# Performance work log

Hardware: AMD Instinct MI355X
Metric: run time of the kernel (lower is better)

The kernel has to match this reference:

```python
import jax, jax.numpy as jnp
import numpy as np

EMBED_DIM = 128
N_CLASSES = 5
NX = 1024
NY = 1024


def setup_inputs() -> dict:
    key = jax.random.key(0)
    k1, k2 = jax.random.split(key)
    z_x = jax.random.normal(k1, (NX, EMBED_DIM), dtype=jnp.float32)
    z_y = jax.random.normal(k2, (NY, EMBED_DIM), dtype=jnp.float32)
    # Parameter init exactly as in __init__ for the L1 compare
    ex = 2 * np.sqrt(2 / np.pi) * EMBED_DIM
    var = 4 * (1 - 2 / np.pi) * EMBED_DIM
    beta_init = ex / np.sqrt(var)
    theta = jnp.ones((1, N_CLASSES - 1), dtype=jnp.float32) / np.sqrt(var)  # clamped >=0, already positive
    beta = jnp.full((N_CLASSES - 1,), beta_init, dtype=jnp.float32)
    return {"z_x": z_x, "z_y": z_y, "theta": theta, "beta": beta}


def reference(z_x, z_y, theta, beta):
    # L1 compare: s[i,j] = -sum_d |z_x[i,d] - z_y[j,d]|   -> (Nx, Ny)
    s = -jnp.sum(jnp.abs(z_x[:, None, :] - z_y[None, :, :]), axis=-1)
    # SSA: dual softmax soft alignment
    a = jax.nn.softmax(s, axis=1)  # row softmax
    b = jax.nn.softmax(s, axis=0)  # column softmax
    a = a + b - a * b
    a = a / jnp.sum(a)
    # weighted reduction -> scalar similarity
    c = jnp.sum(a * s)
    logits = c * theta + beta  # (1, n_classes-1) broadcast
    return logits.reshape(-1)
```

## Files before the change

### kernel.cpp

```cpp
#include <hip/hip_runtime.h>
#include <math.h>

#define NXC 1024
#define NYC 1024
#define DC  128
#define NCM1 4
#define NTILE 256
#define NBLKA 512

#define WS_STILE 0
#define WS_ROWP  524288
#define WS_COLP  589824
#define WS_PART  622592

typedef _Float16 half2v __attribute__((ext_vector_type(2)));
union H2U { half2v h; unsigned u; };

#if defined(__has_builtin)
#if __has_builtin(__builtin_amdgcn_fdot2)
#define HAVE_FDOT2 1
#endif
#endif

__device__ __forceinline__ float absdiff_dot(uint4 xa, uint4 ya, float acc)
{
    const unsigned* xu = (const unsigned*)&xa;
    const unsigned* yu = (const unsigned*)&ya;
    half2v one; one.x = (_Float16)1.f; one.y = (_Float16)1.f;
    #pragma unroll
    for (int q = 0; q < 4; ++q) {
        H2U x, y, d;
        x.u = xu[q]; y.u = yu[q];
        d.h = x.h - y.h;
        d.u &= 0x7FFF7FFFu;
#ifdef HAVE_FDOT2
        acc = __builtin_amdgcn_fdot2(d.h, one, acc, false);
#else
        acc += (float)d.h.x + (float)d.h.y;
#endif
    }
    return acc;
}

__global__ __launch_bounds__(256, 2) void distance_kernel(
    const float* __restrict__ zx, const float* __restrict__ zy,
    float* __restrict__ ws)
{
    __shared__ __align__(16) _Float16 xs[64 * 128];
    __shared__ __align__(16) _Float16 ys[32 * 128];
    __shared__ float cpm[32][32], cpl[32][32];

    _Float16* stile = (_Float16*)(ws + WS_STILE);
    float* rowp  = ws + WS_ROWP;
    float* colp  = ws + WS_COLP;

    const int t    = threadIdx.x;
    const int tile = blockIdx.x >> 1;
    const int h    = blockIdx.x & 1;
    const int bx   = tile & 15;
    const int by   = tile >> 4;
    const int x0   = by * 64;
    const int y0   = bx * 64 + h * 32;

    #pragma unroll
    for (int k = 0; k < 4; ++k) {
        int idx = t + k * 256;
        int r   = idx >> 4;
        int j   = idx & 15;
        int off = r * 128 + 8 * (j ^ ((r >> 2) & 7));
        const float4* gx = (const float4*)(zx + (size_t)(x0 + r) * DC + 8 * j);
        float4 v0 = gx[0], v1 = gx[1];
        uint4 hx;
        {
            H2U a, b, c, d;
            a.h.x = (_Float16)v0.x; a.h.y = (_Float16)v0.y;
            b.h.x = (_Float16)v0.z; b.h.y = (_Float16)v0.w;
            c.h.x = (_Float16)v1.x; c.h.y = (_Float16)v1.y;
            d.h.x = (_Float16)v1.z; d.h.y = (_Float16)v1.w;
            hx.x = a.u; hx.y = b.u; hx.z = c.u; hx.w = d.u;
        }
        *(uint4*)(xs + off) = hx;
    }
    #pragma unroll
    for (int k = 0; k < 2; ++k) {
        int idx = t + k * 256;
        int r   = idx >> 4;
        int j   = idx & 15;
        int off = r * 128 + 8 * (j ^ ((r >> 2) & 7));
        const float4* gy = (const float4*)(zy + (size_t)(y0 + r) * DC + 8 * j);
        float4 v0 = gy[0], v1 = gy[1];
        uint4 hy;
        {
            H2U a, b, c, d;
            a.h.x = (_Float16)v0.x; a.h.y = (_Float16)v0.y;
            b.h.x = (_Float16)v0.z; b.h.y = (_Float16)v0.w;
            c.h.x = (_Float16)v1.x; c.h.y = (_Float16)v1.y;
            d.h.x = (_Float16)v1.z; d.h.y = (_Float16)v1.w;
            hy.x = a.u; hy.y = b.u; hy.z = c.u; hy.w = d.u;
        }
        *(uint4*)(ys + off) = hy;
    }
    __syncthreads();

    const int tx = t & 7;
    const int ty = t >> 3;
    const int xswz = (ty >> 1) & 7;
    const int yswz = tx;

    const _Float16* xb = xs + (2 * ty) * 128;
    const _Float16* yb = ys + (4 * tx) * 128;

    float acc[2][4];
    #pragma unroll
    for (int i = 0; i < 2; ++i)
        #pragma unroll
        for (int j = 0; j < 4; ++j) acc[i][j] = 0.f;

    uint4 xc0 = *(const uint4*)(xb +       8 * (0 ^ xswz));
    uint4 xc1 = *(const uint4*)(xb + 128 + 8 * (0 ^ xswz));
    uint4 yc0 = *(const uint4*)(yb +       8 * (0 ^ yswz));
    uint4 yc1 = *(const uint4*)(yb + 128 + 8 * (0 ^ yswz));
    uint4 yc2 = *(const uint4*)(yb + 256 + 8 * (0 ^ yswz));
    uint4 yc3 = *(const uint4*)(yb + 384 + 8 * (0 ^ yswz));

    #pragma unroll 4
    for (int j = 0; j < 16; ++j) {
        uint4 xa0 = xc0, xa1 = xc1, ya0 = yc0, ya1 = yc1, ya2 = yc2, ya3 = yc3;
        const int jn = (j + 1) & 15;
        xc0 = *(const uint4*)(xb +       8 * (jn ^ xswz));
        xc1 = *(const uint4*)(xb + 128 + 8 * (jn ^ xswz));
        yc0 = *(const uint4*)(yb +       8 * (jn ^ yswz));
        yc1 = *(const uint4*)(yb + 128 + 8 * (jn ^ yswz));
        yc2 = *(const uint4*)(yb + 256 + 8 * (jn ^ yswz));
        yc3 = *(const uint4*)(yb + 384 + 8 * (jn ^ yswz));

        acc[0][0] = absdiff_dot(xa0, ya0, acc[0][0]);
        acc[0][1] = absdiff_dot(xa0, ya1, acc[0][1]);
        acc[0][2] = absdiff_dot(xa0, ya2, acc[0][2]);
        acc[0][3] = absdiff_dot(xa0, ya3, acc[0][3]);
        acc[1][0] = absdiff_dot(xa1, ya0, acc[1][0]);
        acc[1][1] = absdiff_dot(xa1, ya1, acc[1][1]);
        acc[1][2] = absdiff_dot(xa1, ya2, acc[1][2]);
        acc[1][3] = absdiff_dot(xa1, ya3, acc[1][3]);
    }

    float sv[2][4];
    #pragma unroll
    for (int i = 0; i < 2; ++i)
        #pragma unroll
        for (int j = 0; j < 4; ++j) sv[i][j] = -acc[i][j];

    {
        H2U p0, p1, p2, p3;
        p0.h.x = (_Float16)sv[0][0]; p0.h.y = (_Float16)sv[0][1];
        p1.h.x = (_Float16)sv[0][2]; p1.h.y = (_Float16)sv[0][3];
        p2.h.x = (_Float16)sv[1][0]; p2.h.y = (_Float16)sv[1][1];
        p3.h.x = (_Float16)sv[1][2]; p3.h.y = (_Float16)sv[1][3];
        uint4 pk; pk.x = p0.u; pk.y = p1.u; pk.z = p2.u; pk.w = p3.u;
        *(uint4*)(stile + (size_t)tile * 4096 + h * 2048 + t * 8) = pk;
    }

    #pragma unroll
    for (int i = 0; i < 2; ++i) {
        float m = fmaxf(fmaxf(sv[i][0], sv[i][1]), fmaxf(sv[i][2], sv[i][3]));
        float l = __expf(sv[i][0] - m) + __expf(sv[i][1] - m)
                + __expf(sv[i][2] - m) + __expf(sv[i][3] - m);
        #pragma unroll
        for (int off = 1; off < 8; off <<= 1) {
            float mo = __shfl_xor(m, off, 64);
            float lo = __shfl_xor(l, off, 64);
            float nm = fmaxf(m, mo);
            l = l * __expf(m - nm) + lo * __expf(mo - nm);
            m = nm;
        }
        if (tx == 0)
            *(float2*)(rowp + 2 * ((size_t)(x0 + 2 * ty + i) * 32 + bx * 2 + h)) = make_float2(m, l);
    }

    #pragma unroll
    for (int j = 0; j < 4; ++j) {
        float m = fmaxf(sv[0][j], sv[1][j]);
        float l = __expf(sv[0][j] - m) + __expf(sv[1][j] - m);
        cpm[ty][4 * tx + j] = m;
        cpl[ty][4 * tx + j] = l;
    }
    __syncthreads();
    if (t < 32) {
        float m = cpm[0][t], l = cpl[0][t];
        #pragma unroll 8
        for (int k = 1; k < 32; ++k) {
            float mo = cpm[k][t], lo = cpl[k][t];
            float nm = fmaxf(m, mo);
            l = l * __expf(m - nm) + lo * __expf(mo - nm);
            m = nm;
        }
        *(float2*)(colp + 2 * ((size_t)(y0 + t) * 16 + by)) = make_float2(m, l);
    }
}

__global__ __launch_bounds__(512, 2) void reduce_kernel(
    const float* __restrict__ ws_in, float* __restrict__ ws_out)
{
    __shared__ float rm_s[64], rl_s[64], cm_s[64], cl_s[64];
    __shared__ float red0[8], red1[8];

    const _Float16* stile = (const _Float16*)(ws_in + WS_STILE);
    const float4* rowp4 = (const float4*)(ws_in + WS_ROWP);
    const float4* colp4 = (const float4*)(ws_in + WS_COLP);
    float* part = ws_out + WS_PART;

    const int t    = threadIdx.x;
    const int tile = blockIdx.x;
    const int bx   = tile & 15;
    const int by   = tile >> 4;
    const int x0   = by * 64;
    const int y0   = bx * 64;

    uint4 pk = *(const uint4*)(stile + (size_t)tile * 4096 + t * 8);

    const int item  = t >> 3;
    const int lane8 = t & 7;

    {
        float4 q0 = rowp4[(size_t)(x0 + item) * 16 + 2 * lane8];
        float4 q1 = rowp4[(size_t)(x0 + item) * 16 + 2 * lane8 + 1];
        float m = fmaxf(q0.x, q0.z);
        float l = q0.y * __expf(q0.x - m) + q0.w * __expf(q0.z - m);
        float m2 = fmaxf(q1.x, q1.z);
        float l2 = q1.y * __expf(q1.x - m2) + q1.w * __expf(q1.z - m2);
        float nm = fmaxf(m, m2);
        l = l * __expf(m - nm) + l2 * __expf(m2 - nm);
        m = nm;
        #pragma unroll
        for (int off = 1; off < 8; off <<= 1) {
            float mo = __shfl_xor(m, off, 64);
            float lo = __shfl_xor(l, off, 64);
            nm = fmaxf(m, mo);
            l = l * __expf(m - nm) + lo * __expf(mo - nm);
            m = nm;
        }
        if (lane8 == 0) { rm_s[item] = m; rl_s[item] = 1.f / l; }
    }
    {
        float4 q = colp4[(size_t)(y0 + item) * 8 + lane8];
        float m = fmaxf(q.x, q.z);
        float l = q.y * __expf(q.x - m) + q.w * __expf(q.z - m);
        #pragma unroll
        for (int off = 1; off < 8; off <<= 1) {
            float mo = __shfl_xor(m, off, 64);
            float lo = __shfl_xor(l, off, 64);
            float nm = fmaxf(m, mo);
            l = l * __expf(m - nm) + lo * __expf(mo - nm);
            m = nm;
        }
        if (lane8 == 0) { cm_s[item] = m; cl_s[item] = 1.f / l; }
    }
    __syncthreads();

    const int tp = t & 255;
    const int hh = t >> 8;
    const int i0 = 2 * (tp >> 3);
    const int c0 = 32 * hh + 4 * (tp & 7);

    float sv[2][4];
    {
        H2U u0, u1, u2, u3;
        u0.u = pk.x; u1.u = pk.y; u2.u = pk.z; u3.u = pk.w;
        sv[0][0] = (float)u0.h.x; sv[0][1] = (float)u0.h.y;
        sv[0][2] = (float)u1.h.x; sv[0][3] = (float)u1.h.y;
        sv[1][0] = (float)u2.h.x; sv[1][1] = (float)u2.h.y;
        sv[1][2] = (float)u3.h.x; sv[1][3] = (float)u3.h.y;
    }

    float S0 = 0.f, S1 = 0.f;
    #pragma unroll
    for (int i = 0; i < 2; ++i) {
        const float rm = rm_s[i0 + i];
        const float rl = rl_s[i0 + i];
        #pragma unroll
        for (int j = 0; j < 4; ++j) {
            const float cm = cm_s[c0 + j];
            const float cl = cl_s[c0 + j];
            float s = sv[i][j];
            float a = __expf(s - rm) * rl;
            float b = __expf(s - cm) * cl;
            float w = a + b - a * b;
            S0 += w;
            S1 += w * s;
        }
    }
    #pragma unroll
    for (int off = 32; off; off >>= 1) {
        S0 += __shfl_xor(S0, off, 64);
        S1 += __shfl_xor(S1, off, 64);
    }
    {
        const int wave = t >> 6, lane = t & 63;
        if (lane == 0) { red0[wave] = S0; red1[wave] = S1; }
    }
    __syncthreads();
    if (t == 0) {
        float t0 = 0.f, t1 = 0.f;
        #pragma unroll
        for (int w = 0; w < 8; ++w) { t0 += red0[w]; t1 += red1[w]; }
        *(float2*)(part + 2 * tile) = make_float2(t0, t1);
    }
}

__global__ __launch_bounds__(256) void finalize_kernel(
    const float* __restrict__ ws,
    const float* __restrict__ theta, const float* __restrict__ beta,
    float* __restrict__ out)
{
    __shared__ float red0[4], red1[4];
    const float* part = ws + WS_PART;
    const int t = threadIdx.x;

    float2 p = ((const float2*)part)[t];
    float S0 = p.x, S1 = p.y;
    #pragma unroll
    for (int off = 32; off; off >>= 1) {
        S0 += __shfl_xor(S0, off, 64);
        S1 += __shfl_xor(S1, off, 64);
    }
    const int wave = t >> 6, lane = t & 63;
    if (lane == 0) { red0[wave] = S0; red1[wave] = S1; }
    __syncthreads();
    if (t < NCM1) {
        float t0 = red0[0] + red0[1] + red0[2] + red0[3];
        float t1 = red1[0] + red1[1] + red1[2] + red1[3];
        float c = t1 / t0;
        out[t] = c * theta[t] + beta[t];
    }
}

extern "C" void kernel_launch(void* const* d_in, const int* in_sizes, int n_in,
                              void* d_out, int out_size, void* d_ws, size_t ws_size,
                              hipStream_t stream)
{
    const float* zx    = (const float*)d_in[0];
    const float* zy    = (const float*)d_in[1];
    const float* theta = (const float*)d_in[2];
    const float* beta  = (const float*)d_in[3];
    float* out = (float*)d_out;
    float* ws  = (float*)d_ws;

    distance_kernel<<<NBLKA, 256, 0, stream>>>(zx, zy, ws);
    reduce_kernel<<<NTILE, 512, 0, stream>>>(ws, ws);
    finalize_kernel<<<1, 256, 0, stream>>>(ws, theta, beta, out);
}
```

Baseline: 76.20 us.

## Fuse distance, reduce and finalize into one persistent kernel with grid barriers

Merges the three kernels into a single 256-block, 512-thread kernel that keeps the score tile in registers across a software grid barrier, which removes the half-precision score-tile round trip through global memory and two kernel launch gaps. Each block now covers a full 64x64 tile, so the row partials shrink to 16 per row. A second grid barrier lets block 0 do the final reduction. The design relies on all 256 blocks being co-resident, which 256 CUs make plausible; otherwise it deadlocks. The barrier adds atomic and spin cost.

```diff
diff --git a/kernel.cpp b/kernel.cpp
--- a/kernel.cpp
+++ b/kernel.cpp
@@ -6,12 +6,10 @@
 #define DC  128
 #define NCM1 4
 #define NTILE 256
-#define NBLKA 512
-
-#define WS_STILE 0
-#define WS_ROWP  524288
-#define WS_COLP  589824
-#define WS_PART  622592
+
+#define WS_ROWP  0
+#define WS_COLP  65536
+#define WS_PART  131072
 
 typedef _Float16 half2v __attribute__((ext_vector_type(2)));
 union H2U { half2v h; unsigned u; };
@@ -21,6 +19,35 @@
 #define HAVE_FDOT2 1
 #endif
 #endif
+
+__device__ unsigned g_bar_count = 0;
+__device__ unsigned g_bar_gen   = 0;
+
+__device__ __forceinline__ void grid_barrier(unsigned nblk)
+{
+    __syncthreads();
+    if (threadIdx.x == 0) {
+        __threadfence();
+        unsigned my = __hip_atomic_load(&g_bar_gen, __ATOMIC_RELAXED,
+                                        __HIP_MEMORY_SCOPE_AGENT);
+        unsigned prev = __hip_atomic_fetch_add(&g_bar_count, 1u,
+                                               __ATOMIC_ACQ_REL,
+                                               __HIP_MEMORY_SCOPE_AGENT);
+        if (prev == nblk - 1u) {
+            __hip_atomic_store(&g_bar_count, 0u, __ATOMIC_RELAXED,
+                               __HIP_MEMORY_SCOPE_AGENT);
+            __hip_atomic_store(&g_bar_gen, my + 1u, __ATOMIC_RELEASE,
+                               __HIP_MEMORY_SCOPE_AGENT);
+        } else {
+            while (__hip_atomic_load(&g_bar_gen, __ATOMIC_ACQUIRE,
+                                     __HIP_MEMORY_SCOPE_AGENT) == my) {
+                __builtin_amdgcn_s_sleep(2);
+            }
+        }
+        __threadfence();
+    }
+    __syncthreads();
+}
 
 __device__ __forceinline__ float absdiff_dot(uint4 xa, uint4 ya, float acc)
 {
@@ -42,29 +69,31 @@
     return acc;
 }
 
-__global__ __launch_bounds__(256, 2) void distance_kernel(
+__global__ __launch_bounds__(512, 1) void ssa_fused_kernel(
     const float* __restrict__ zx, const float* __restrict__ zy,
-    float* __restrict__ ws)
+    const float* __restrict__ theta, const float* __restrict__ beta,
+    float* __restrict__ ws, float* __restrict__ out)
 {
     __shared__ __align__(16) _Float16 xs[64 * 128];
-    __shared__ __align__(16) _Float16 ys[32 * 128];
-    __shared__ float cpm[32][32], cpl[32][32];
-
-    _Float16* stile = (_Float16*)(ws + WS_STILE);
-    float* rowp  = ws + WS_ROWP;
-    float* colp  = ws + WS_COLP;
+    __shared__ __align__(16) _Float16 ys[64 * 128];
+    __shared__ float cpm[32][65], cpl[32][65];
+    __shared__ float rm_s[64], rl_s[64], cm_s[64], cl_s[64];
+    __shared__ float red0[8], red1[8];
+
+    float* rowp = ws + WS_ROWP;
+    float* colp = ws + WS_COLP;
+    float* part = ws + WS_PART;
 
     const int t    = threadIdx.x;
-    const int tile = blockIdx.x >> 1;
-    const int h    = blockIdx.x & 1;
+    const int tile = blockIdx.x;
     const int bx   = tile & 15;
     const int by   = tile >> 4;
     const int x0   = by * 64;
-    const int y0   = bx * 64 + h * 32;
-
-    #pragma unroll
-    for (int k = 0; k < 4; ++k) {
-        int idx = t + k * 256;
+    const int y0   = bx * 64;
+
+    #pragma unroll
+    for (int k = 0; k < 2; ++k) {
+        int idx = t + k * 512;
         int r   = idx >> 4;
         int j   = idx & 15;
         int off = r * 128 + 8 * (j ^ ((r >> 2) & 7));
@@ -83,7 +112,7 @@
     }
     #pragma unroll
     for (int k = 0; k < 2; ++k) {
-        int idx = t + k * 256;
+        int idx = t + k * 512;
         int r   = idx >> 4;
         int j   = idx & 15;
         int off = r * 128 + 8 * (j ^ ((r >> 2) & 7));
@@ -102,10 +131,10 @@
     }
     __syncthreads();
 
-    const int tx = t & 7;
-    const int ty = t >> 3;
+    const int tx = t & 15;
+    const int ty = t >> 4;
     const int xswz = (ty >> 1) & 7;
-    const int yswz = tx;
+    const int yswz = tx & 7;
 
     const _Float16* xb = xs + (2 * ty) * 128;
     const _Float16* yb = ys + (4 * tx) * 128;
@@ -150,23 +179,13 @@
         #pragma unroll
         for (int j = 0; j < 4; ++j) sv[i][j] = -acc[i][j];
 
-    {
-        H2U p0, p1, p2, p3;
-        p0.h.x = (_Float16)sv[0][0]; p0.h.y = (_Float16)sv[0][1];
-        p1.h.x = (_Float16)sv[0][2]; p1.h.y = (_Float16)sv[0][3];
-        p2.h.x = (_Float16)sv[1][0]; p2.h.y = (_Float16)sv[1][1];
-        p3.h.x = (_Float16)sv[1][2]; p3.h.y = (_Float16)sv[1][3];
-        uint4 pk; pk.x = p0.u; pk.y = p1.u; pk.z = p2.u; pk.w = p3.u;
-        *(uint4*)(stile + (size_t)tile * 4096 + h * 2048 + t * 8) = pk;
-    }
-
     #pragma unroll
     for (int i = 0; i < 2; ++i) {
         float m = fmaxf(fmaxf(sv[i][0], sv[i][1]), fmaxf(sv[i][2], sv[i][3]));
         float l = __expf(sv[i][0] - m) + __expf(sv[i][1] - m)
                 + __expf(sv[i][2] - m) + __expf(sv[i][3] - m);
         #pragma unroll
-        for (int off = 1; off < 8; off <<= 1) {
+        for (int off = 1; off < 16; off <<= 1) {
             float mo = __shfl_xor(m, off, 64);
             float lo = __shfl_xor(l, off, 64);
             float nm = fmaxf(m, mo);
@@ -174,7 +193,7 @@
             m = nm;
         }
         if (tx == 0)
-            *(float2*)(rowp + 2 * ((size_t)(x0 + 2 * ty + i) * 32 + bx * 2 + h)) = make_float2(m, l);
+            *(float2*)(rowp + 2 * ((size_t)(x0 + 2 * ty + i) * 16 + bx)) = make_float2(m, l);
     }
 
     #pragma unroll
@@ -185,7 +204,7 @@
         cpl[ty][4 * tx + j] = l;
     }
     __syncthreads();
-    if (t < 32) {
+    if (t < 64) {
         float m = cpm[0][t], l = cpl[0][t];
         #pragma unroll 8
         for (int k = 1; k < 32; ++k) {
@@ -196,53 +215,13 @@
         }
         *(float2*)(colp + 2 * ((size_t)(y0 + t) * 16 + by)) = make_float2(m, l);
     }
-}
-
-__global__ __launch_bounds__(512, 2) void reduce_kernel(
-    const float* __restrict__ ws_in, float* __restrict__ ws_out)
-{
-    __shared__ float rm_s[64], rl_s[64], cm_s[64], cl_s[64];
-    __shared__ float red0[8], red1[8];
-
-    const _Float16* stile = (const _Float16*)(ws_in + WS_STILE);
-    const float4* rowp4 = (const float4*)(ws_in + WS_ROWP);
-    const float4* colp4 = (const float4*)(ws_in + WS_COLP);
-    float* part = ws_out + WS_PART;
-
-    const int t    = threadIdx.x;
-    const int tile = blockIdx.x;
-    const int bx   = tile & 15;
-    const int by   = tile >> 4;
-    const int x0   = by * 64;
-    const int y0   = bx * 64;
-
-    uint4 pk = *(const uint4*)(stile + (size_t)tile * 4096 + t * 8);
+
+    grid_barrier(NTILE);
 
     const int item  = t >> 3;
     const int lane8 = t & 7;
-
     {
-        float4 q0 = rowp4[(size_t)(x0 + item) * 16 + 2 * lane8];
-        float4 q1 = rowp4[(size_t)(x0 + item) * 16 + 2 * lane8 + 1];
-        float m = fmaxf(q0.x, q0.z);
-        float l = q0.y * __expf(q0.x - m) + q0.w * __expf(q0.z - m);
-        float m2 = fmaxf(q1.x, q1.z);
-        float l2 = q1.y * __expf(q1.x - m2) + q1.w * __expf(q1.z - m2);
-        float nm = fmaxf(m, m2);
-        l = l * __expf(m - nm) + l2 * __expf(m2 - nm);
-        m = nm;
-        #pragma unroll
-        for (int off = 1; off < 8; off <<= 1) {
-            float mo = __shfl_xor(m, off, 64);
-            float lo = __shfl_xor(l, off, 64);
-            nm = fmaxf(m, mo);
-            l = l * __expf(m - nm) + lo * __expf(mo - nm);
-            m = nm;
-        }
-        if (lane8 == 0) { rm_s[item] = m; rl_s[item] = 1.f / l; }
-    }
-    {
-        float4 q = colp4[(size_t)(y0 + item) * 8 + lane8];
+        float4 q = ((const float4*)rowp)[(size_t)(x0 + item) * 8 + lane8];
         float m = fmaxf(q.x, q.z);
         float l = q.y * __expf(q.x - m) + q.w * __expf(q.z - m);
         #pragma unroll
@@ -253,34 +232,33 @@
             l = l * __expf(m - nm) + lo * __expf(mo - nm);
             m = nm;
         }
+        if (lane8 == 0) { rm_s[item] = m; rl_s[item] = 1.f / l; }
+    }
+    {
+        float4 q = ((const float4*)colp)[(size_t)(y0 + item) * 8 + lane8];
+        float m = fmaxf(q.x, q.z);
+        float l = q.y * __expf(q.x - m) + q.w * __expf(q.z - m);
+        #pragma unroll
+        for (int off = 1; off < 8; off <<= 1) {
+            float mo = __shfl_xor(m, off, 64);
+            float lo = __shfl_xor(l, off, 64);
+            float nm = fmaxf(m, mo);
+            l = l * __expf(m - nm) + lo * __expf(mo - nm);
+            m = nm;
+        }
         if (lane8 == 0) { cm_s[item] = m; cl_s[item] = 1.f / l; }
     }
     __syncthreads();
 
-    const int tp = t & 255;
-    const int hh = t >> 8;
-    const int i0 = 2 * (tp >> 3);
-    const int c0 = 32 * hh + 4 * (tp & 7);
-
-    float sv[2][4];
-    {
-        H2U u0, u1, u2, u3;
-        u0.u = pk.x; u1.u = pk.y; u2.u = pk.z; u3.u = pk.w;
-        sv[0][0] = (float)u0.h.x; sv[0][1] = (float)u0.h.y;
-        sv[0][2] = (float)u1.h.x; sv[0][3] = (float)u1.h.y;
-        sv[1][0] = (float)u2.h.x; sv[1][1] = (float)u2.h.y;
-        sv[1][2] = (float)u3.h.x; sv[1][3] = (float)u3.h.y;
-    }
-
     float S0 = 0.f, S1 = 0.f;
     #pragma unroll
     for (int i = 0; i < 2; ++i) {
-        const float rm = rm_s[i0 + i];
-        const float rl = rl_s[i0 + i];
+        const float rm = rm_s[2 * ty + i];
+        const float rl = rl_s[2 * ty + i];
         #pragma unroll
         for (int j = 0; j < 4; ++j) {
-            const float cm = cm_s[c0 + j];
-            const float cl = cl_s[c0 + j];
+            const float cm = cm_s[4 * tx + j];
+            const float cl = cl_s[4 * tx + j];
             float s = sv[i][j];
             float a = __expf(s - rm) * rl;
             float b = __expf(s - cm) * cl;
@@ -294,10 +272,7 @@
         S0 += __shfl_xor(S0, off, 64);
         S1 += __shfl_xor(S1, off, 64);
     }
-    {
-        const int wave = t >> 6, lane = t & 63;
-        if (lane == 0) { red0[wave] = S0; red1[wave] = S1; }
-    }
+    if ((t & 63) == 0) { red0[t >> 6] = S0; red1[t >> 6] = S1; }
     __syncthreads();
     if (t == 0) {
         float t0 = 0.f, t1 = 0.f;
@@ -305,32 +280,29 @@
         for (int w = 0; w < 8; ++w) { t0 += red0[w]; t1 += red1[w]; }
         *(float2*)(part + 2 * tile) = make_float2(t0, t1);
     }
-}
-
-__global__ __launch_bounds__(256) void finalize_kernel(
-    const float* __restrict__ ws,
-    const float* __restrict__ theta, const float* __restrict__ beta,
-    float* __restrict__ out)
-{
-    __shared__ float red0[4], red1[4];
-    const float* part = ws + WS_PART;
-    const int t = threadIdx.x;
-
-    float2 p = ((const float2*)part)[t];
-    float S0 = p.x, S1 = p.y;
-    #pragma unroll
-    for (int off = 32; off; off >>= 1) {
-        S0 += __shfl_xor(S0, off, 64);
-        S1 += __shfl_xor(S1, off, 64);
-    }
-    const int wave = t >> 6, lane = t & 63;
-    if (lane == 0) { red0[wave] = S0; red1[wave] = S1; }
-    __syncthreads();
-    if (t < NCM1) {
-        float t0 = red0[0] + red0[1] + red0[2] + red0[3];
-        float t1 = red1[0] + red1[1] + red1[2] + red1[3];
-        float c = t1 / t0;
-        out[t] = c * theta[t] + beta[t];
+
+    grid_barrier(NTILE);
+
+    if (blockIdx.x == 0) {
+        float P0 = 0.f, P1 = 0.f;
+        if (t < NTILE) {
+            float2 p = ((const float2*)part)[t];
+            P0 = p.x; P1 = p.y;
+        }
+        #pragma unroll
+        for (int off = 32; off; off >>= 1) {
+            P0 += __shfl_xor(P0, off, 64);
+            P1 += __shfl_xor(P1, off, 64);
+        }
+        if ((t & 63) == 0) { red0[t >> 6] = P0; red1[t >> 6] = P1; }
+        __syncthreads();
+        if (t < NCM1) {
+            float t0 = 0.f, t1 = 0.f;
+            #pragma unroll
+            for (int w = 0; w < 8; ++w) { t0 += red0[w]; t1 += red1[w]; }
+            float c = t1 / t0;
+            out[t] = c * theta[t] + beta[t];
+        }
     }
 }
 
@@ -345,7 +317,5 @@
     float* out = (float*)d_out;
     float* ws  = (float*)d_ws;
 
-    distance_kernel<<<NBLKA, 256, 0, stream>>>(zx, zy, ws);
-    reduce_kernel<<<NTILE, 512, 0, stream>>>(ws, ws);
-    finalize_kernel<<<1, 256, 0, stream>>>(ws, theta, beta, out);
+    ssa_fused_kernel<<<NTILE, 512, 0, stream>>>(zx, zy, theta, beta, ws, out);
 }
```

Result: slower. 125.6 us (+64.9%).
